# Kernel optimization log

Measured on AMD Instinct MI355X. Metric: run time of the kernel, lower is better.

## Reference

```python
import jax, jax.numpy as jnp
import numpy as np

N = 100000      # nodes
E = 3200000     # edges
F_IN = 1433     # Cora num_node_features
H = 16          # hidden channels
C = 7           # Cora num_classes


def setup_inputs() -> dict:
    key = jax.random.key(0)
    ks = jax.random.split(key, 8)
    x = jax.random.normal(ks[0], (N, F_IN), dtype=jnp.float32)
    edge_index = jax.random.randint(ks[1], (2, E), 0, N, dtype=jnp.int64)
    W1 = jax.random.normal(ks[2], (F_IN, H), dtype=jnp.float32) * (1.0 / np.sqrt(F_IN))
    b1 = jnp.zeros((H,), dtype=jnp.float32)
    W2 = jax.random.normal(ks[3], (H, H), dtype=jnp.float32) * (1.0 / np.sqrt(H))
    b2 = jnp.zeros((H,), dtype=jnp.float32)
    W3 = jax.random.normal(ks[4], (H, C), dtype=jnp.float32) * (1.0 / np.sqrt(H))
    b3 = jnp.zeros((C,), dtype=jnp.float32)
    return {"x": x, "W1": W1, "b1": b1, "W2": W2, "b2": b2,
            "W3": W3, "b3": b3, "edge_index": edge_index}


def reference(x, W1, b1, W2, b2, W3, b3, edge_index):
    # Add self loops (GCNConv default) and compute symmetric normalization once;
    # it is identical for all three layers.
    loop = jnp.arange(N, dtype=edge_index.dtype)
    src = jnp.concatenate([edge_index[0], loop])
    dst = jnp.concatenate([edge_index[1], loop])
    deg = jax.ops.segment_sum(jnp.ones_like(dst, dtype=x.dtype), dst, num_segments=N)
    dinv = jnp.where(deg > 0, jax.lax.rsqrt(deg), 0.0)
    norm = dinv[src] * dinv[dst]  # [E+N]

    def conv(h, W, b):
        h = h @ W                                   # [N, out]
        msg = h[src] * norm[:, None]                # gather + scale, [E+N, out]
        return jax.ops.segment_sum(msg, dst, num_segments=N) + b

    h = jax.nn.relu(conv(x, W1, b1))
    h = jax.nn.relu(conv(h, W2, b2))
    logits = conv(h, W3, b3)
    return jax.nn.log_softmax(logits, axis=1)
```

## Files before the change

kernel.cpp:

```cpp
#include <hip/hip_runtime.h>
#include <hip/hip_fp16.h>

#define F_IN 1433
#define BCAP 96
#define WSTR 2048


typedef _Float16 f16x8 __attribute__((ext_vector_type(8)));
typedef float    f32x4 __attribute__((ext_vector_type(4)));

__global__ __launch_bounds__(256) void k_prep(const float* __restrict__ W1,
    int* __restrict__ cnt, _Float16* __restrict__ wt, int N)
{
    int i = blockIdx.x * 256 + threadIdx.x;
    if (i < N) cnt[i] = 0;
    if (i < 16 * WSTR) {
        int c = i >> 11, k = i & (WSTR - 1);
        float v = (k < F_IN) ? W1[k * 16 + c] : 0.0f;
        wt[i] = (_Float16)v;
    }
}

__global__ __launch_bounds__(256) void k_scatter(const int* __restrict__ ei,
    int* cnt, int* bucket, int E, int N)
{
    int e = blockIdx.x * 256 + threadIdx.x;
    if (e < E) {
        int s = ei[e], d = ei[E + e];
        if ((unsigned)s < (unsigned)N && (unsigned)d < (unsigned)N) {
            int slot = atomicAdd(&cnt[d], 1);
            if (slot < BCAP) bucket[(size_t)d * BCAP + slot] = s;
        }
    }
}

__global__ __launch_bounds__(256, 4) void k_gemm(
    const float* __restrict__ x, const _Float16* __restrict__ wt,
    const int* __restrict__ cnt, float* __restrict__ s, int N)
{
    int tid = threadIdx.x;
    int wv = tid >> 6, lane = tid & 63;
    int ntiles = (N + 15) >> 4;
    int tile = blockIdx.x * 4 + wv;
    if (tile >= ntiles) return;

    int rc = lane & 15;
    int g  = lane >> 4;
    int row = tile * 16 + rc;
    const float* xr = x + (size_t)((row < N) ? row : (N - 1)) * F_IN;
    const _Float16* wrow = wt + (rc << 11);

    struct __attribute__((packed, aligned(4))) f4u { float f[4]; };

    f32x4 acc = {0.0f, 0.0f, 0.0f, 0.0f};
    int kb = g * 8;

    #pragma unroll 4
    for (int ch = 0; ch < 44; ++ch) {
        int k0 = ch * 32 + kb;
        f4u xa = *(const f4u*)&xr[k0];
        f4u xb = *(const f4u*)&xr[k0 + 4];
        f16x8 bv = *(const f16x8*)&wrow[k0];
        f16x8 av;
        #pragma unroll
        for (int j = 0; j < 4; ++j) {
            av[j]     = (_Float16)xa.f[j];
            av[j + 4] = (_Float16)xb.f[j];
        }
        acc = __builtin_amdgcn_mfma_f32_16x16x32_f16(av, bv, acc, 0, 0, 0);
    }
    {
        int k0 = 1408 + kb;
        f16x8 av, bv;
        bv = *(const f16x8*)&wrow[k0];
        #pragma unroll
        for (int j = 0; j < 8; ++j) {
            int k = k0 + j;
            av[j] = (_Float16)((k < F_IN) ? xr[k] : 0.0f);
        }
        acc = __builtin_amdgcn_mfma_f32_16x16x32_f16(av, bv, acc, 0, 0, 0);
    }

    #pragma unroll
    for (int r = 0; r < 4; ++r) {
        int grow = tile * 16 + g * 4 + r;
        if (grow < N) {
            float di = rsqrtf((float)cnt[grow] + 1.0f);
            s[grow * 16 + rc] = acc[r] * di;
        }
    }
}

__global__ __launch_bounds__(256) void k_aggA(
    const int* __restrict__ cnt, const int* __restrict__ bucket,
    const float* __restrict__ sin, const float* __restrict__ W,
    const float* __restrict__ bias, float* __restrict__ sout, int N)
{
    __shared__ float w[256], bs[16];
    int tid = threadIdx.x;
    w[tid] = W[tid];
    if (tid < 16) bs[tid] = bias[tid];
    __syncthreads();

    int wave = tid >> 6, lane = tid & 63;
    int dst = blockIdx.x * 4 + wave;
    if (dst >= N) return;
    int g = lane >> 4, c = lane & 15;
    int deg = min(cnt[dst], BCAP);
    const int* bk = bucket + (size_t)dst * BCAP;

    int e0 = (lane < deg)      ? bk[lane]      : 0;
    int e1 = (64 + lane < deg) ? bk[64 + lane] : 0;

    float acc = (g == 0) ? sin[dst * 16 + c] : 0.0f;
    for (int base = 0; base < deg; base += 32) {
        float vs = 0.0f;
        #pragma unroll
        for (int i = 0; i < 8; ++i) {
            int j = base + g + 4 * i;
            int sa = __shfl(e0, j & 63, 64), sb = __shfl(e1, j & 63, 64);
            int sv = (j < 64) ? sa : sb;
            float v = (j < deg) ? sin[sv * 16 + c] : 0.0f;
            vs += v;
        }
        acc += vs;
    }
    acc += __shfl_xor(acc, 16, 64);
    acc += __shfl_xor(acc, 32, 64);

    float di = rsqrtf((float)cnt[dst] + 1.0f);
    float h = fmaxf(fmaf(di, acc, bs[c]), 0.0f);
    float t = 0.0f;
    #pragma unroll
    for (int k = 0; k < 16; ++k)
        t = fmaf(__shfl(h, k, 16), w[k * 16 + c], t);
    if (lane < 16) sout[dst * 16 + c] = di * t;
}

__global__ __launch_bounds__(256) void k_aggB(
    const int* __restrict__ cnt, const int* __restrict__ bucket,
    const float* __restrict__ sin, const float* __restrict__ W,
    const float* __restrict__ bias, float* __restrict__ sout, int N)
{
    __shared__ float w[112], bs[16];
    int tid = threadIdx.x;
    if (tid < 112) w[tid] = W[tid];
    if (tid < 16) bs[tid] = bias[tid];
    __syncthreads();

    int wave = tid >> 6, lane = tid & 63;
    int dst = blockIdx.x * 4 + wave;
    if (dst >= N) return;
    int g = lane >> 4, c = lane & 15;
    int deg = min(cnt[dst], BCAP);
    const int* bk = bucket + (size_t)dst * BCAP;

    int e0 = (lane < deg)      ? bk[lane]      : 0;
    int e1 = (64 + lane < deg) ? bk[64 + lane] : 0;

    float acc = (g == 0) ? sin[dst * 16 + c] : 0.0f;
    for (int base = 0; base < deg; base += 32) {
        float vs = 0.0f;
        #pragma unroll
        for (int i = 0; i < 8; ++i) {
            int j = base + g + 4 * i;
            int sa = __shfl(e0, j & 63, 64), sb = __shfl(e1, j & 63, 64);
            int sv = (j < 64) ? sa : sb;
            float v = (j < deg) ? sin[sv * 16 + c] : 0.0f;
            vs += v;
        }
        acc += vs;
    }
    acc += __shfl_xor(acc, 16, 64);
    acc += __shfl_xor(acc, 32, 64);

    float di = rsqrtf((float)cnt[dst] + 1.0f);
    float h = fmaxf(fmaf(di, acc, bs[c]), 0.0f);
    int cc = (c < 7) ? c : 0;
    float t = 0.0f;
    #pragma unroll
    for (int k = 0; k < 16; ++k)
        t = fmaf(__shfl(h, k, 16), w[k * 7 + cc], t);
    if (lane < 7) sout[dst * 7 + c] = di * t;
}

__global__ __launch_bounds__(256) void k_aggC(
    const int* __restrict__ cnt, const int* __restrict__ bucket,
    const float* __restrict__ sin, const float* __restrict__ bias,
    float* __restrict__ out, int N)
{
    __shared__ float bs[8];
    int tid = threadIdx.x;
    if (tid < 7) bs[tid] = bias[tid];
    if (tid == 7) bs[7] = 0.0f;
    __syncthreads();

    int wave = tid >> 6, lane = tid & 63;
    int dst = blockIdx.x * 4 + wave;
    if (dst >= N) return;
    int g8 = lane >> 3, c8 = lane & 7;
    bool c7 = (c8 < 7);
    int cc = c7 ? c8 : 0;
    int deg = min(cnt[dst], BCAP);
    const int* bk = bucket + (size_t)dst * BCAP;

    int e0 = (lane < deg)      ? bk[lane]      : 0;
    int e1 = (64 + lane < deg) ? bk[64 + lane] : 0;

    float acc = (g8 == 0 && c7) ? sin[dst * 7 + c8] : 0.0f;
    for (int base = 0; base < deg; base += 64) {
        float vs = 0.0f;
        #pragma unroll
        for (int i = 0; i < 8; ++i) {
            int j = base + g8 + 8 * i;
            int sa = __shfl(e0, j & 63, 64), sb = __shfl(e1, j & 63, 64);
            int sv = (j < 64) ? sa : sb;
            float v = (j < deg && c7) ? sin[sv * 7 + cc] : 0.0f;
            vs += v;
        }
        acc += vs;
    }
    acc += __shfl_xor(acc, 8, 64);
    acc += __shfl_xor(acc, 16, 64);
    acc += __shfl_xor(acc, 32, 64);

    if (lane < 8) {
        float di = rsqrtf((float)cnt[dst] + 1.0f);
        float logit = c7 ? fmaf(di, acc, bs[c8]) : -1e30f;
        float m = logit;
        m = fmaxf(m, __shfl_xor(m, 1, 8));
        m = fmaxf(m, __shfl_xor(m, 2, 8));
        m = fmaxf(m, __shfl_xor(m, 4, 8));
        float e = c7 ? expf(logit - m) : 0.0f;
        float ssum = e;
        ssum += __shfl_xor(ssum, 1, 8);
        ssum += __shfl_xor(ssum, 2, 8);
        ssum += __shfl_xor(ssum, 4, 8);
        if (c7) out[dst * 7 + c8] = logit - m - logf(ssum);
    }
}

extern "C" void kernel_launch(void* const* d_in, const int* in_sizes, int n_in,
                              void* d_out, int out_size, void* d_ws, size_t ws_size,
                              hipStream_t stream)
{
    const float* x  = (const float*)d_in[0];
    const float* W1 = (const float*)d_in[1];
    const float* b1 = (const float*)d_in[2];
    const float* W2 = (const float*)d_in[3];
    const float* b2 = (const float*)d_in[4];
    const float* W3 = (const float*)d_in[5];
    const float* b3 = (const float*)d_in[6];
    const int*   ei = (const int*)d_in[7];
    float* out = (float*)d_out;

    int N = in_sizes[0] / F_IN;
    int E = in_sizes[7] / 2;

    int*      cnt    = (int*)d_ws;
    int*      bucket = cnt + N;
    _Float16* wt     = (_Float16*)(bucket + (size_t)N * BCAP);
    float*    s1     = (float*)(wt + 16 * WSTR);
    float*    s2     = s1 + 16 * (size_t)N;
    float*    s3     = s2 + 16 * (size_t)N;

    int nbN = (N + 255) / 256;
    int nbE = (E + 255) / 256;
    int nb4 = (N + 3) / 4;
    int ntiles = (N + 15) / 16;
    int nbG = (ntiles + 3) / 4;

    k_prep   <<<nbN, 256, 0, stream>>>(W1, cnt, wt, N);
    k_scatter<<<nbE, 256, 0, stream>>>(ei, cnt, bucket, E, N);
    k_gemm   <<<nbG, 256, 0, stream>>>(x, wt, cnt, s1, N);
    k_aggA   <<<nb4, 256, 0, stream>>>(cnt, bucket, s1, W2, b1, s2, N);
    k_aggB   <<<nb4, 256, 0, stream>>>(cnt, bucket, s2, W3, b2, s3, N);
    k_aggC   <<<nb4, 256, 0, stream>>>(cnt, bucket, s3, b3, out, N);
}
```

Baseline: 504.2 us.

## Fuse all stages into one persistent kernel with software grid barriers

Replaces the five separate launches (scatter, gemm, three aggregation layers) with one persistent kernel sized to the device's resident block count. Stages are separated by atomic-counter grid barriers. The GEMM now runs before the edge scatter, so the degree scaling of s1 moves into a separate elementwise pass after the first barrier. This removes launch gaps and lets the x-streaming GEMM and the atomic scatter run in the same kernel. The cost is barrier spin overhead, an extra pass over s1, a lower occupancy cap from launch bounds, and a host-side device-property query on every call.

```diff
diff --git a/kernel.cpp b/kernel.cpp
--- a/kernel.cpp
+++ b/kernel.cpp
@@ -10,233 +10,213 @@
 typedef float    f32x4 __attribute__((ext_vector_type(4)));
 
 __global__ __launch_bounds__(256) void k_prep(const float* __restrict__ W1,
-    int* __restrict__ cnt, _Float16* __restrict__ wt, int N)
+    int* __restrict__ bar, int* __restrict__ cnt, _Float16* __restrict__ wt, int N)
 {
     int i = blockIdx.x * 256 + threadIdx.x;
+    if (i < 16) bar[i] = 0;
     if (i < N) cnt[i] = 0;
     if (i < 16 * WSTR) {
         int c = i >> 11, k = i & (WSTR - 1);
-        float v = (k < F_IN) ? W1[k * 16 + c] : 0.0f;
-        wt[i] = (_Float16)v;
-    }
-}
-
-__global__ __launch_bounds__(256) void k_scatter(const int* __restrict__ ei,
-    int* cnt, int* bucket, int E, int N)
+        wt[i] = (_Float16)((k < F_IN) ? W1[k * 16 + c] : 0.0f);
+    }
+}
+
+__device__ __forceinline__ void gridbar(int* bar, int target) {
+    __syncthreads();
+    if (threadIdx.x == 0) {
+        __hip_atomic_fetch_add(bar, 1, __ATOMIC_RELEASE, __HIP_MEMORY_SCOPE_AGENT);
+        while (__hip_atomic_load(bar, __ATOMIC_RELAXED, __HIP_MEMORY_SCOPE_AGENT) < target)
+            __builtin_amdgcn_s_sleep(32);
+        (void)__hip_atomic_load(bar, __ATOMIC_ACQUIRE, __HIP_MEMORY_SCOPE_AGENT);
+    }
+    __syncthreads();
+}
+
+__global__ __launch_bounds__(256, 6) void k_all(
+    const float* __restrict__ x, const _Float16* __restrict__ wt,
+    const int* __restrict__ ei, int* __restrict__ cnt, int* __restrict__ bucket,
+    float* __restrict__ s1, float* __restrict__ s2, float* __restrict__ s3,
+    float* __restrict__ out,
+    const float* __restrict__ W2, const float* __restrict__ b1,
+    const float* __restrict__ W3, const float* __restrict__ b2,
+    const float* __restrict__ b3, int* bar, int N, int E)
 {
-    int e = blockIdx.x * 256 + threadIdx.x;
-    if (e < E) {
-        int s = ei[e], d = ei[E + e];
-        if ((unsigned)s < (unsigned)N && (unsigned)d < (unsigned)N) {
+    __shared__ float w2s[256], w3s[112], b1s[16], b2s[16], b3s[8];
+    int tid = threadIdx.x;
+    w2s[tid] = W2[tid];
+    if (tid < 112) w3s[tid] = W3[tid];
+    if (tid < 16)  b1s[tid] = b1[tid];
+    if (tid < 16)  b2s[tid] = b2[tid];
+    if (tid < 8)   b3s[tid] = (tid < 7) ? b3[tid] : 0.0f;
+    __syncthreads();
+
+    int G = gridDim.x;
+    int wv = tid >> 6, lane = tid & 63;
+    int gw = blockIdx.x * 4 + wv, ngw = G * 4;
+    int gt = blockIdx.x * 256 + tid, ngt = G * 256;
+
+    struct __attribute__((packed, aligned(4))) f4u { float f[4]; };
+
+    {
+        int rc = lane & 15, g = lane >> 4;
+        int kb = g * 8;
+        int ntiles = (N + 15) >> 4;
+        const _Float16* wrow = wt + (rc << 11);
+        for (int tile = gw; tile < ntiles; tile += ngw) {
+            int row = tile * 16 + rc;
+            const float* xr = x + (size_t)((row < N) ? row : (N - 1)) * F_IN;
+            f32x4 acc = {0.0f, 0.0f, 0.0f, 0.0f};
+            #pragma unroll 4
+            for (int ch = 0; ch < 44; ++ch) {
+                int k0 = ch * 32 + kb;
+                f4u xa = *(const f4u*)&xr[k0];
+                f4u xb = *(const f4u*)&xr[k0 + 4];
+                f16x8 bv = *(const f16x8*)&wrow[k0];
+                f16x8 av;
+                #pragma unroll
+                for (int j = 0; j < 4; ++j) {
+                    av[j]     = (_Float16)xa.f[j];
+                    av[j + 4] = (_Float16)xb.f[j];
+                }
+                acc = __builtin_amdgcn_mfma_f32_16x16x32_f16(av, bv, acc, 0, 0, 0);
+            }
+            {
+                int k0 = 1408 + kb;
+                f16x8 av, bv;
+                bv = *(const f16x8*)&wrow[k0];
+                #pragma unroll
+                for (int j = 0; j < 8; ++j) {
+                    int k = k0 + j;
+                    av[j] = (_Float16)((k < F_IN) ? xr[k] : 0.0f);
+                }
+                acc = __builtin_amdgcn_mfma_f32_16x16x32_f16(av, bv, acc, 0, 0, 0);
+            }
+            #pragma unroll
+            for (int r = 0; r < 4; ++r) {
+                int grow = tile * 16 + g * 4 + r;
+                if (grow < N) s1[grow * 16 + rc] = acc[r];
+            }
+        }
+    }
+
+    for (int e = gt; e < E; e += ngt) {
+        int sv = ei[e], d = ei[E + e];
+        if ((unsigned)sv < (unsigned)N && (unsigned)d < (unsigned)N) {
             int slot = atomicAdd(&cnt[d], 1);
-            if (slot < BCAP) bucket[(size_t)d * BCAP + slot] = s;
-        }
-    }
-}
-
-__global__ __launch_bounds__(256, 4) void k_gemm(
-    const float* __restrict__ x, const _Float16* __restrict__ wt,
-    const int* __restrict__ cnt, float* __restrict__ s, int N)
-{
-    int tid = threadIdx.x;
-    int wv = tid >> 6, lane = tid & 63;
-    int ntiles = (N + 15) >> 4;
-    int tile = blockIdx.x * 4 + wv;
-    if (tile >= ntiles) return;
-
-    int rc = lane & 15;
-    int g  = lane >> 4;
-    int row = tile * 16 + rc;
-    const float* xr = x + (size_t)((row < N) ? row : (N - 1)) * F_IN;
-    const _Float16* wrow = wt + (rc << 11);
-
-    struct __attribute__((packed, aligned(4))) f4u { float f[4]; };
-
-    f32x4 acc = {0.0f, 0.0f, 0.0f, 0.0f};
-    int kb = g * 8;
-
-    #pragma unroll 4
-    for (int ch = 0; ch < 44; ++ch) {
-        int k0 = ch * 32 + kb;
-        f4u xa = *(const f4u*)&xr[k0];
-        f4u xb = *(const f4u*)&xr[k0 + 4];
-        f16x8 bv = *(const f16x8*)&wrow[k0];
-        f16x8 av;
+            if (slot < BCAP) bucket[(size_t)d * BCAP + slot] = sv;
+        }
+    }
+
+    gridbar(bar, G);
+
+    for (int i = gt; i < N * 16; i += ngt)
+        s1[i] *= rsqrtf((float)cnt[i >> 4] + 1.0f);
+
+    gridbar(bar, 2 * G);
+
+    int g = lane >> 4, c = lane & 15;
+
+    for (int dst = gw; dst < N; dst += ngw) {
+        int deg = min(cnt[dst], BCAP);
+        const int* bk = bucket + (size_t)dst * BCAP;
+        int e0 = (lane < deg)      ? bk[lane]      : 0;
+        int e1 = (64 + lane < deg) ? bk[64 + lane] : 0;
+        float acc = (g == 0) ? s1[dst * 16 + c] : 0.0f;
+        for (int base = 0; base < deg; base += 32) {
+            float vs = 0.0f;
+            #pragma unroll
+            for (int i = 0; i < 8; ++i) {
+                int j = base + g + 4 * i;
+                int sa = __shfl(e0, j & 63, 64), sb = __shfl(e1, j & 63, 64);
+                int sv = (j < 64) ? sa : sb;
+                float v = (j < deg) ? s1[sv * 16 + c] : 0.0f;
+                vs += v;
+            }
+            acc += vs;
+        }
+        acc += __shfl_xor(acc, 16, 64);
+        acc += __shfl_xor(acc, 32, 64);
+        float di = rsqrtf((float)cnt[dst] + 1.0f);
+        float h = fmaxf(fmaf(di, acc, b1s[c]), 0.0f);
+        float t = 0.0f;
         #pragma unroll
-        for (int j = 0; j < 4; ++j) {
-            av[j]     = (_Float16)xa.f[j];
-            av[j + 4] = (_Float16)xb.f[j];
-        }
-        acc = __builtin_amdgcn_mfma_f32_16x16x32_f16(av, bv, acc, 0, 0, 0);
-    }
-    {
-        int k0 = 1408 + kb;
-        f16x8 av, bv;
-        bv = *(const f16x8*)&wrow[k0];
+        for (int k = 0; k < 16; ++k)
+            t = fmaf(__shfl(h, k, 16), w2s[k * 16 + c], t);
+        if (lane < 16) s2[dst * 16 + c] = di * t;
+    }
+
+    gridbar(bar, 3 * G);
+
+    for (int dst = gw; dst < N; dst += ngw) {
+        int deg = min(cnt[dst], BCAP);
+        const int* bk = bucket + (size_t)dst * BCAP;
+        int e0 = (lane < deg)      ? bk[lane]      : 0;
+        int e1 = (64 + lane < deg) ? bk[64 + lane] : 0;
+        float acc = (g == 0) ? s2[dst * 16 + c] : 0.0f;
+        for (int base = 0; base < deg; base += 32) {
+            float vs = 0.0f;
+            #pragma unroll
+            for (int i = 0; i < 8; ++i) {
+                int j = base + g + 4 * i;
+                int sa = __shfl(e0, j & 63, 64), sb = __shfl(e1, j & 63, 64);
+                int sv = (j < 64) ? sa : sb;
+                float v = (j < deg) ? s2[sv * 16 + c] : 0.0f;
+                vs += v;
+            }
+            acc += vs;
+        }
+        acc += __shfl_xor(acc, 16, 64);
+        acc += __shfl_xor(acc, 32, 64);
+        float di = rsqrtf((float)cnt[dst] + 1.0f);
+        float h = fmaxf(fmaf(di, acc, b2s[c]), 0.0f);
+        int cc = (c < 7) ? c : 0;
+        float t = 0.0f;
         #pragma unroll
-        for (int j = 0; j < 8; ++j) {
-            int k = k0 + j;
-            av[j] = (_Float16)((k < F_IN) ? xr[k] : 0.0f);
-        }
-        acc = __builtin_amdgcn_mfma_f32_16x16x32_f16(av, bv, acc, 0, 0, 0);
-    }
-
-    #pragma unroll
-    for (int r = 0; r < 4; ++r) {
-        int grow = tile * 16 + g * 4 + r;
-        if (grow < N) {
-            float di = rsqrtf((float)cnt[grow] + 1.0f);
-            s[grow * 16 + rc] = acc[r] * di;
-        }
-    }
-}
-
-__global__ __launch_bounds__(256) void k_aggA(
-    const int* __restrict__ cnt, const int* __restrict__ bucket,
-    const float* __restrict__ sin, const float* __restrict__ W,
-    const float* __restrict__ bias, float* __restrict__ sout, int N)
-{
-    __shared__ float w[256], bs[16];
-    int tid = threadIdx.x;
-    w[tid] = W[tid];
-    if (tid < 16) bs[tid] = bias[tid];
-    __syncthreads();
-
-    int wave = tid >> 6, lane = tid & 63;
-    int dst = blockIdx.x * 4 + wave;
-    if (dst >= N) return;
-    int g = lane >> 4, c = lane & 15;
-    int deg = min(cnt[dst], BCAP);
-    const int* bk = bucket + (size_t)dst * BCAP;
-
-    int e0 = (lane < deg)      ? bk[lane]      : 0;
-    int e1 = (64 + lane < deg) ? bk[64 + lane] : 0;
-
-    float acc = (g == 0) ? sin[dst * 16 + c] : 0.0f;
-    for (int base = 0; base < deg; base += 32) {
-        float vs = 0.0f;
-        #pragma unroll
-        for (int i = 0; i < 8; ++i) {
-            int j = base + g + 4 * i;
-            int sa = __shfl(e0, j & 63, 64), sb = __shfl(e1, j & 63, 64);
-            int sv = (j < 64) ? sa : sb;
-            float v = (j < deg) ? sin[sv * 16 + c] : 0.0f;
-            vs += v;
-        }
-        acc += vs;
-    }
-    acc += __shfl_xor(acc, 16, 64);
-    acc += __shfl_xor(acc, 32, 64);
-
-    float di = rsqrtf((float)cnt[dst] + 1.0f);
-    float h = fmaxf(fmaf(di, acc, bs[c]), 0.0f);
-    float t = 0.0f;
-    #pragma unroll
-    for (int k = 0; k < 16; ++k)
-        t = fmaf(__shfl(h, k, 16), w[k * 16 + c], t);
-    if (lane < 16) sout[dst * 16 + c] = di * t;
-}
-
-__global__ __launch_bounds__(256) void k_aggB(
-    const int* __restrict__ cnt, const int* __restrict__ bucket,
-    const float* __restrict__ sin, const float* __restrict__ W,
-    const float* __restrict__ bias, float* __restrict__ sout, int N)
-{
-    __shared__ float w[112], bs[16];
-    int tid = threadIdx.x;
-    if (tid < 112) w[tid] = W[tid];
-    if (tid < 16) bs[tid] = bias[tid];
-    __syncthreads();
-
-    int wave = tid >> 6, lane = tid & 63;
-    int dst = blockIdx.x * 4 + wave;
-    if (dst >= N) return;
-    int g = lane >> 4, c = lane & 15;
-    int deg = min(cnt[dst], BCAP);
-    const int* bk = bucket + (size_t)dst * BCAP;
-
-    int e0 = (lane < deg)      ? bk[lane]      : 0;
-    int e1 = (64 + lane < deg) ? bk[64 + lane] : 0;
-
-    float acc = (g == 0) ? sin[dst * 16 + c] : 0.0f;
-    for (int base = 0; base < deg; base += 32) {
-        float vs = 0.0f;
-        #pragma unroll
-        for (int i = 0; i < 8; ++i) {
-            int j = base + g + 4 * i;
-            int sa = __shfl(e0, j & 63, 64), sb = __shfl(e1, j & 63, 64);
-            int sv = (j < 64) ? sa : sb;
-            float v = (j < deg) ? sin[sv * 16 + c] : 0.0f;
-            vs += v;
-        }
-        acc += vs;
-    }
-    acc += __shfl_xor(acc, 16, 64);
-    acc += __shfl_xor(acc, 32, 64);
-
-    float di = rsqrtf((float)cnt[dst] + 1.0f);
-    float h = fmaxf(fmaf(di, acc, bs[c]), 0.0f);
-    int cc = (c < 7) ? c : 0;
-    float t = 0.0f;
-    #pragma unroll
-    for (int k = 0; k < 16; ++k)
-        t = fmaf(__shfl(h, k, 16), w[k * 7 + cc], t);
-    if (lane < 7) sout[dst * 7 + c] = di * t;
-}
-
-__global__ __launch_bounds__(256) void k_aggC(
-    const int* __restrict__ cnt, const int* __restrict__ bucket,
-    const float* __restrict__ sin, const float* __restrict__ bias,
-    float* __restrict__ out, int N)
-{
-    __shared__ float bs[8];
-    int tid = threadIdx.x;
-    if (tid < 7) bs[tid] = bias[tid];
-    if (tid == 7) bs[7] = 0.0f;
-    __syncthreads();
-
-    int wave = tid >> 6, lane = tid & 63;
-    int dst = blockIdx.x * 4 + wave;
-    if (dst >= N) return;
+        for (int k = 0; k < 16; ++k)
+            t = fmaf(__shfl(h, k, 16), w3s[k * 7 + cc], t);
+        if (lane < 7) s3[dst * 7 + c] = di * t;
+    }
+
+    gridbar(bar, 4 * G);
+
     int g8 = lane >> 3, c8 = lane & 7;
     bool c7 = (c8 < 7);
-    int cc = c7 ? c8 : 0;
-    int deg = min(cnt[dst], BCAP);
-    const int* bk = bucket + (size_t)dst * BCAP;
-
-    int e0 = (lane < deg)      ? bk[lane]      : 0;
-    int e1 = (64 + lane < deg) ? bk[64 + lane] : 0;
-
-    float acc = (g8 == 0 && c7) ? sin[dst * 7 + c8] : 0.0f;
-    for (int base = 0; base < deg; base += 64) {
-        float vs = 0.0f;
-        #pragma unroll
-        for (int i = 0; i < 8; ++i) {
-            int j = base + g8 + 8 * i;
-            int sa = __shfl(e0, j & 63, 64), sb = __shfl(e1, j & 63, 64);
-            int sv = (j < 64) ? sa : sb;
-            float v = (j < deg && c7) ? sin[sv * 7 + cc] : 0.0f;
-            vs += v;
-        }
-        acc += vs;
-    }
-    acc += __shfl_xor(acc, 8, 64);
-    acc += __shfl_xor(acc, 16, 64);
-    acc += __shfl_xor(acc, 32, 64);
-
-    if (lane < 8) {
-        float di = rsqrtf((float)cnt[dst] + 1.0f);
-        float logit = c7 ? fmaf(di, acc, bs[c8]) : -1e30f;
-        float m = logit;
-        m = fmaxf(m, __shfl_xor(m, 1, 8));
-        m = fmaxf(m, __shfl_xor(m, 2, 8));
-        m = fmaxf(m, __shfl_xor(m, 4, 8));
-        float e = c7 ? expf(logit - m) : 0.0f;
-        float ssum = e;
-        ssum += __shfl_xor(ssum, 1, 8);
-        ssum += __shfl_xor(ssum, 2, 8);
-        ssum += __shfl_xor(ssum, 4, 8);
-        if (c7) out[dst * 7 + c8] = logit - m - logf(ssum);
+    int cc8 = c7 ? c8 : 0;
+    for (int dst = gw; dst < N; dst += ngw) {
+        int deg = min(cnt[dst], BCAP);
+        const int* bk = bucket + (size_t)dst * BCAP;
+        int e0 = (lane < deg)      ? bk[lane]      : 0;
+        int e1 = (64 + lane < deg) ? bk[64 + lane] : 0;
+        float acc = (g8 == 0 && c7) ? s3[dst * 7 + c8] : 0.0f;
+        for (int base = 0; base < deg; base += 64) {
+            float vs = 0.0f;
+            #pragma unroll
+            for (int i = 0; i < 8; ++i) {
+                int j = base + g8 + 8 * i;
+                int sa = __shfl(e0, j & 63, 64), sb = __shfl(e1, j & 63, 64);
+                int sv = (j < 64) ? sa : sb;
+                float v = (j < deg && c7) ? s3[sv * 7 + cc8] : 0.0f;
+                vs += v;
+            }
+            acc += vs;
+        }
+        acc += __shfl_xor(acc, 8, 64);
+        acc += __shfl_xor(acc, 16, 64);
+        acc += __shfl_xor(acc, 32, 64);
+        if (lane < 8) {
+            float di = rsqrtf((float)cnt[dst] + 1.0f);
+            float logit = c7 ? fmaf(di, acc, b3s[c8]) : -1e30f;
+            float m = logit;
+            m = fmaxf(m, __shfl_xor(m, 1, 8));
+            m = fmaxf(m, __shfl_xor(m, 2, 8));
+            m = fmaxf(m, __shfl_xor(m, 4, 8));
+            float e = c7 ? expf(logit - m) : 0.0f;
+            float ssum = e;
+            ssum += __shfl_xor(ssum, 1, 8);
+            ssum += __shfl_xor(ssum, 2, 8);
+            ssum += __shfl_xor(ssum, 4, 8);
+            if (c7) out[dst * 7 + c8] = logit - m - logf(ssum);
+        }
     }
 }
 
@@ -257,7 +237,8 @@
     int N = in_sizes[0] / F_IN;
     int E = in_sizes[7] / 2;
 
-    int*      cnt    = (int*)d_ws;
+    int*      bar    = (int*)d_ws;
+    int*      cnt    = bar + 16;
     int*      bucket = cnt + N;
     _Float16* wt     = (_Float16*)(bucket + (size_t)N * BCAP);
     float*    s1     = (float*)(wt + 16 * WSTR);
@@ -265,15 +246,16 @@
     float*    s3     = s2 + 16 * (size_t)N;
 
     int nbN = (N + 255) / 256;
-    int nbE = (E + 255) / 256;
-    int nb4 = (N + 3) / 4;
-    int ntiles = (N + 15) / 16;
-    int nbG = (ntiles + 3) / 4;
-
-    k_prep   <<<nbN, 256, 0, stream>>>(W1, cnt, wt, N);
-    k_scatter<<<nbE, 256, 0, stream>>>(ei, cnt, bucket, E, N);
-    k_gemm   <<<nbG, 256, 0, stream>>>(x, wt, cnt, s1, N);
-    k_aggA   <<<nb4, 256, 0, stream>>>(cnt, bucket, s1, W2, b1, s2, N);
-    k_aggB   <<<nb4, 256, 0, stream>>>(cnt, bucket, s2, W3, b2, s3, N);
-    k_aggC   <<<nb4, 256, 0, stream>>>(cnt, bucket, s3, b3, out, N);
-}
+    k_prep<<<nbN, 256, 0, stream>>>(W1, bar, cnt, wt, N);
+
+    int dev = 0, numCU = 256, occ = 6;
+    hipGetDevice(&dev);
+    hipDeviceProp_t props;
+    if (hipGetDeviceProperties(&props, dev) == hipSuccess) numCU = props.multiProcessorCount;
+    if (hipOccupancyMaxActiveBlocksPerMultiprocessor(&occ, k_all, 256, 0) != hipSuccess || occ < 1)
+        occ = 1;
+    int grid = numCU * occ;
+
+    k_all<<<grid, 256, 0, stream>>>(x, wt, ei, cnt, bucket, s1, s2, s3, out,
+                                    W2, b1, W3, b2, b3, bar, N, E);
+}
```

Measured after the change: 822.4 us. +63.1%, slower.

## Stage x tile in LDS as fp16 and split K across waves

Applied to the files above, without the earlier changes.

The first-layer GEMM now has each block own one 16-row tile. It loads that tile's x rows with coalesced row-contiguous reads, converts them to fp16 into shared memory, and splits the K loop across the four waves. Partial MFMA accumulators are combined with a shared-memory reduction before degree scaling. This replaces strided per-lane global reads with coalesced loads. In exchange it needs about 50KB of LDS per block, which lowers occupancy, and adds two barriers per block.

```diff
diff --git a/kernel.cpp b/kernel.cpp
--- a/kernel.cpp
+++ b/kernel.cpp
@@ -4,6 +4,7 @@
 #define F_IN 1433
 #define BCAP 96
 #define WSTR 2048
+#define XSTR 1448
 
 
 typedef _Float16 f16x8 __attribute__((ext_vector_type(8)));
@@ -34,60 +35,73 @@
     }
 }
 
-__global__ __launch_bounds__(256, 4) void k_gemm(
+__global__ __launch_bounds__(256) void k_gemm(
     const float* __restrict__ x, const _Float16* __restrict__ wt,
     const int* __restrict__ cnt, float* __restrict__ s, int N)
 {
-    int tid = threadIdx.x;
-    int wv = tid >> 6, lane = tid & 63;
+    __shared__ _Float16 xs[16 * XSTR];
+    __shared__ float red[4 * 256];
+
+    int tid = threadIdx.x;
+    int w = tid >> 6, lane = tid & 63;
+    int tile = blockIdx.x;
     int ntiles = (N + 15) >> 4;
-    int tile = blockIdx.x * 4 + wv;
     if (tile >= ntiles) return;
+
+    struct __attribute__((packed, aligned(4))) f4u { float f[4]; };
+
+    #pragma unroll
+    for (int r = 0; r < 4; ++r) {
+        int rr = w * 4 + r;
+        int grow = tile * 16 + rr;
+        const float* xr = x + (size_t)((grow < N) ? grow : (N - 1)) * F_IN;
+        #pragma unroll
+        for (int it = 0; it < 6; ++it) {
+            int k4 = it * 256 + lane * 4;
+            if (k4 < XSTR) {
+                _Float16 h4[4];
+                if (k4 + 4 <= F_IN) {
+                    f4u v = *(const f4u*)&xr[k4];
+                    #pragma unroll
+                    for (int j = 0; j < 4; ++j) h4[j] = (_Float16)v.f[j];
+                } else {
+                    #pragma unroll
+                    for (int j = 0; j < 4; ++j) {
+                        int k = k4 + j;
+                        h4[j] = (_Float16)((k < F_IN) ? xr[k] : 0.0f);
+                    }
+                }
+                *(__attribute__((ext_vector_type(4))) _Float16*)&xs[rr * XSTR + k4] =
+                    *(__attribute__((ext_vector_type(4))) _Float16*)h4;
+            }
+        }
+    }
+    __syncthreads();
 
     int rc = lane & 15;
     int g  = lane >> 4;
-    int row = tile * 16 + rc;
-    const float* xr = x + (size_t)((row < N) ? row : (N - 1)) * F_IN;
+    int kb = g * 8;
     const _Float16* wrow = wt + (rc << 11);
-
-    struct __attribute__((packed, aligned(4))) f4u { float f[4]; };
+    const _Float16* xrow = xs + rc * XSTR;
 
     f32x4 acc = {0.0f, 0.0f, 0.0f, 0.0f};
-    int kb = g * 8;
-
-    #pragma unroll 4
-    for (int ch = 0; ch < 44; ++ch) {
+    for (int ch = w; ch < 45; ch += 4) {
         int k0 = ch * 32 + kb;
-        f4u xa = *(const f4u*)&xr[k0];
-        f4u xb = *(const f4u*)&xr[k0 + 4];
+        f16x8 av = *(const f16x8*)&xrow[k0];
         f16x8 bv = *(const f16x8*)&wrow[k0];
-        f16x8 av;
-        #pragma unroll
-        for (int j = 0; j < 4; ++j) {
-            av[j]     = (_Float16)xa.f[j];
-            av[j + 4] = (_Float16)xb.f[j];
-        }
         acc = __builtin_amdgcn_mfma_f32_16x16x32_f16(av, bv, acc, 0, 0, 0);
     }
-    {
-        int k0 = 1408 + kb;
-        f16x8 av, bv;
-        bv = *(const f16x8*)&wrow[k0];
-        #pragma unroll
-        for (int j = 0; j < 8; ++j) {
-            int k = k0 + j;
-            av[j] = (_Float16)((k < F_IN) ? xr[k] : 0.0f);
-        }
-        acc = __builtin_amdgcn_mfma_f32_16x16x32_f16(av, bv, acc, 0, 0, 0);
-    }
-
-    #pragma unroll
-    for (int r = 0; r < 4; ++r) {
-        int grow = tile * 16 + g * 4 + r;
-        if (grow < N) {
-            float di = rsqrtf((float)cnt[grow] + 1.0f);
-            s[grow * 16 + rc] = acc[r] * di;
-        }
+
+    #pragma unroll
+    for (int q = 0; q < 4; ++q)
+        red[w * 256 + (g * 4 + q) * 16 + rc] = acc[q];
+    __syncthreads();
+
+    int row = tile * 16 + (tid >> 4);
+    if (row < N) {
+        float v = red[tid] + red[256 + tid] + red[512 + tid] + red[768 + tid];
+        float di = rsqrtf((float)cnt[row] + 1.0f);
+        s[row * 16 + (tid & 15)] = v * di;
     }
 }
 
@@ -268,11 +282,10 @@
     int nbE = (E + 255) / 256;
     int nb4 = (N + 3) / 4;
     int ntiles = (N + 15) / 16;
-    int nbG = (ntiles + 3) / 4;
 
     k_prep   <<<nbN, 256, 0, stream>>>(W1, cnt, wt, N);
     k_scatter<<<nbE, 256, 0, stream>>>(ei, cnt, bucket, E, N);
-    k_gemm   <<<nbG, 256, 0, stream>>>(x, wt, cnt, s1, N);
+    k_gemm   <<<ntiles, 256, 0, stream>>>(x, wt, cnt, s1, N);
     k_aggA   <<<nb4, 256, 0, stream>>>(cnt, bucket, s1, W2, b1, s2, N);
     k_aggB   <<<nb4, 256, 0, stream>>>(cnt, bucket, s2, W3, b2, s3, N);
     k_aggC   <<<nb4, 256, 0, stream>>>(cnt, bucket, s3, b3, out, N);
```

Result: slower. 535.0 us (+6.1%).

## Merge GEMM and edge scatter into one launch, defer degree scaling to aggregation

Applied to the files above, without the earlier changes.

The layer-1 GEMM and the edge bucketing scatter now run as disjoint block ranges of a single kernel, so the compute-heavy feature transform can overlap the atomic-bound scatter. This is possible because the GEMM no longer needs degree counts: it writes unscaled features, and the first aggregation applies rsqrt(deg) per source neighbour on the fly. In exchange that aggregation does an extra gather of cnt for every edge. The aggregation kernels also process four destinations per wave instead of one, which cuts the block count.

```diff
diff --git a/kernel.cpp b/kernel.cpp
--- a/kernel.cpp
+++ b/kernel.cpp
@@ -21,79 +21,75 @@
     }
 }
 
-__global__ __launch_bounds__(256) void k_scatter(const int* __restrict__ ei,
-    int* cnt, int* bucket, int E, int N)
-{
-    int e = blockIdx.x * 256 + threadIdx.x;
-    if (e < E) {
-        int s = ei[e], d = ei[E + e];
-        if ((unsigned)s < (unsigned)N && (unsigned)d < (unsigned)N) {
-            int slot = atomicAdd(&cnt[d], 1);
-            if (slot < BCAP) bucket[(size_t)d * BCAP + slot] = s;
-        }
-    }
-}
-
-__global__ __launch_bounds__(256, 4) void k_gemm(
+__global__ __launch_bounds__(256) void k_ms(
     const float* __restrict__ x, const _Float16* __restrict__ wt,
-    const int* __restrict__ cnt, float* __restrict__ s, int N)
-{
-    int tid = threadIdx.x;
-    int wv = tid >> 6, lane = tid & 63;
-    int ntiles = (N + 15) >> 4;
-    int tile = blockIdx.x * 4 + wv;
-    if (tile >= ntiles) return;
-
-    int rc = lane & 15;
-    int g  = lane >> 4;
-    int row = tile * 16 + rc;
-    const float* xr = x + (size_t)((row < N) ? row : (N - 1)) * F_IN;
-    const _Float16* wrow = wt + (rc << 11);
-
-    struct __attribute__((packed, aligned(4))) f4u { float f[4]; };
-
-    f32x4 acc = {0.0f, 0.0f, 0.0f, 0.0f};
-    int kb = g * 8;
-
-    #pragma unroll 4
-    for (int ch = 0; ch < 44; ++ch) {
-        int k0 = ch * 32 + kb;
-        f4u xa = *(const f4u*)&xr[k0];
-        f4u xb = *(const f4u*)&xr[k0 + 4];
-        f16x8 bv = *(const f16x8*)&wrow[k0];
-        f16x8 av;
+    const int* __restrict__ ei, int* __restrict__ cnt, int* __restrict__ bucket,
+    float* __restrict__ g1, int nbG, int N, int E)
+{
+    int tid = threadIdx.x;
+    if ((int)blockIdx.x < nbG) {
+        int wv = tid >> 6, lane = tid & 63;
+        int ntiles = (N + 15) >> 4;
+        int tile = blockIdx.x * 4 + wv;
+        if (tile >= ntiles) return;
+
+        int rc = lane & 15;
+        int g  = lane >> 4;
+        int row = tile * 16 + rc;
+        const float* xr = x + (size_t)((row < N) ? row : (N - 1)) * F_IN;
+        const _Float16* wrow = wt + (rc << 11);
+
+        struct __attribute__((packed, aligned(4))) f4u { float f[4]; };
+
+        f32x4 acc = {0.0f, 0.0f, 0.0f, 0.0f};
+        int kb = g * 8;
+
+        #pragma unroll 4
+        for (int ch = 0; ch < 44; ++ch) {
+            int k0 = ch * 32 + kb;
+            f4u xa = *(const f4u*)&xr[k0];
+            f4u xb = *(const f4u*)&xr[k0 + 4];
+            f16x8 bv = *(const f16x8*)&wrow[k0];
+            f16x8 av;
+            #pragma unroll
+            for (int j = 0; j < 4; ++j) {
+                av[j]     = (_Float16)xa.f[j];
+                av[j + 4] = (_Float16)xb.f[j];
+            }
+            acc = __builtin_amdgcn_mfma_f32_16x16x32_f16(av, bv, acc, 0, 0, 0);
+        }
+        {
+            int k0 = 1408 + kb;
+            f16x8 av, bv;
+            bv = *(const f16x8*)&wrow[k0];
+            #pragma unroll
+            for (int j = 0; j < 8; ++j) {
+                int k = k0 + j;
+                av[j] = (_Float16)((k < F_IN) ? xr[k] : 0.0f);
+            }
+            acc = __builtin_amdgcn_mfma_f32_16x16x32_f16(av, bv, acc, 0, 0, 0);
+        }
+
         #pragma unroll
-        for (int j = 0; j < 4; ++j) {
-            av[j]     = (_Float16)xa.f[j];
-            av[j + 4] = (_Float16)xb.f[j];
-        }
-        acc = __builtin_amdgcn_mfma_f32_16x16x32_f16(av, bv, acc, 0, 0, 0);
-    }
-    {
-        int k0 = 1408 + kb;
-        f16x8 av, bv;
-        bv = *(const f16x8*)&wrow[k0];
-        #pragma unroll
-        for (int j = 0; j < 8; ++j) {
-            int k = k0 + j;
-            av[j] = (_Float16)((k < F_IN) ? xr[k] : 0.0f);
-        }
-        acc = __builtin_amdgcn_mfma_f32_16x16x32_f16(av, bv, acc, 0, 0, 0);
-    }
-
-    #pragma unroll
-    for (int r = 0; r < 4; ++r) {
-        int grow = tile * 16 + g * 4 + r;
-        if (grow < N) {
-            float di = rsqrtf((float)cnt[grow] + 1.0f);
-            s[grow * 16 + rc] = acc[r] * di;
+        for (int r = 0; r < 4; ++r) {
+            int grow = tile * 16 + g * 4 + r;
+            if (grow < N) g1[grow * 16 + rc] = acc[r];
+        }
+    } else {
+        int e = ((int)blockIdx.x - nbG) * 256 + tid;
+        if (e < E) {
+            int s = ei[e], d = ei[E + e];
+            if ((unsigned)s < (unsigned)N && (unsigned)d < (unsigned)N) {
+                int slot = atomicAdd(&cnt[d], 1);
+                if (slot < BCAP) bucket[(size_t)d * BCAP + slot] = s;
+            }
         }
     }
 }
 
 __global__ __launch_bounds__(256) void k_aggA(
     const int* __restrict__ cnt, const int* __restrict__ bucket,
-    const float* __restrict__ sin, const float* __restrict__ W,
+    const float* __restrict__ g1, const float* __restrict__ W,
     const float* __restrict__ bias, float* __restrict__ sout, int N)
 {
     __shared__ float w[256], bs[16];
@@ -103,38 +99,45 @@
     __syncthreads();
 
     int wave = tid >> 6, lane = tid & 63;
-    int dst = blockIdx.x * 4 + wave;
-    if (dst >= N) return;
     int g = lane >> 4, c = lane & 15;
-    int deg = min(cnt[dst], BCAP);
-    const int* bk = bucket + (size_t)dst * BCAP;
-
-    int e0 = (lane < deg)      ? bk[lane]      : 0;
-    int e1 = (64 + lane < deg) ? bk[64 + lane] : 0;
-
-    float acc = (g == 0) ? sin[dst * 16 + c] : 0.0f;
-    for (int base = 0; base < deg; base += 32) {
-        float vs = 0.0f;
+    int base0 = blockIdx.x * 16 + wave * 4;
+
+    for (int it = 0; it < 4; ++it) {
+        int dst = base0 + it;
+        if (dst >= N) break;
+        int cd = cnt[dst];
+        int deg = min(cd, BCAP);
+        float di = rsqrtf((float)cd + 1.0f);
+        const int* bk = bucket + (size_t)dst * BCAP;
+
+        int e0 = (lane < deg)      ? bk[lane]      : 0;
+        int e1 = (64 + lane < deg) ? bk[64 + lane] : 0;
+
+        float acc = (g == 0) ? di * g1[dst * 16 + c] : 0.0f;
+        for (int base = 0; base < deg; base += 32) {
+            float vs = 0.0f;
+            #pragma unroll
+            for (int i = 0; i < 8; ++i) {
+                int j = base + g + 4 * i;
+                int sa = __shfl(e0, j & 63, 64), sb = __shfl(e1, j & 63, 64);
+                int sv = (j < 64) ? sa : sb;
+                float v = 0.0f;
+                if (j < deg)
+                    v = rsqrtf((float)cnt[sv] + 1.0f) * g1[sv * 16 + c];
+                vs += v;
+            }
+            acc += vs;
+        }
+        acc += __shfl_xor(acc, 16, 64);
+        acc += __shfl_xor(acc, 32, 64);
+
+        float h = fmaxf(fmaf(di, acc, bs[c]), 0.0f);
+        float t = 0.0f;
         #pragma unroll
-        for (int i = 0; i < 8; ++i) {
-            int j = base + g + 4 * i;
-            int sa = __shfl(e0, j & 63, 64), sb = __shfl(e1, j & 63, 64);
-            int sv = (j < 64) ? sa : sb;
-            float v = (j < deg) ? sin[sv * 16 + c] : 0.0f;
-            vs += v;
-        }
-        acc += vs;
-    }
-    acc += __shfl_xor(acc, 16, 64);
-    acc += __shfl_xor(acc, 32, 64);
-
-    float di = rsqrtf((float)cnt[dst] + 1.0f);
-    float h = fmaxf(fmaf(di, acc, bs[c]), 0.0f);
-    float t = 0.0f;
-    #pragma unroll
-    for (int k = 0; k < 16; ++k)
-        t = fmaf(__shfl(h, k, 16), w[k * 16 + c], t);
-    if (lane < 16) sout[dst * 16 + c] = di * t;
+        for (int k = 0; k < 16; ++k)
+            t = fmaf(__shfl(h, k, 16), w[k * 16 + c], t);
+        if (lane < 16) sout[dst * 16 + c] = di * t;
+    }
 }
 
 __global__ __launch_bounds__(256) void k_aggB(
@@ -149,39 +152,44 @@
     __syncthreads();
 
     int wave = tid >> 6, lane = tid & 63;
-    int dst = blockIdx.x * 4 + wave;
-    if (dst >= N) return;
     int g = lane >> 4, c = lane & 15;
-    int deg = min(cnt[dst], BCAP);
-    const int* bk = bucket + (size_t)dst * BCAP;
-
-    int e0 = (lane < deg)      ? bk[lane]      : 0;
-    int e1 = (64 + lane < deg) ? bk[64 + lane] : 0;
-
-    float acc = (g == 0) ? sin[dst * 16 + c] : 0.0f;
-    for (int base = 0; base < deg; base += 32) {
-        float vs = 0.0f;
+    int base0 = blockIdx.x * 16 + wave * 4;
+
+    for (int it = 0; it < 4; ++it) {
+        int dst = base0 + it;
+        if (dst >= N) break;
+        int cd = cnt[dst];
+        int deg = min(cd, BCAP);
+        float di = rsqrtf((float)cd + 1.0f);
+        const int* bk = bucket + (size_t)dst * BCAP;
+
+        int e0 = (lane < deg)      ? bk[lane]      : 0;
+        int e1 = (64 + lane < deg) ? bk[64 + lane] : 0;
+
+        float acc = (g == 0) ? sin[dst * 16 + c] : 0.0f;
+        for (int base = 0; base < deg; base += 32) {
+            float vs = 0.0f;
+            #pragma unroll
+            for (int i = 0; i < 8; ++i) {
+                int j = base + g + 4 * i;
+                int sa = __shfl(e0, j & 63, 64), sb = __shfl(e1, j & 63, 64);
+                int sv = (j < 64) ? sa : sb;
+                float v = (j < deg) ? sin[sv * 16 + c] : 0.0f;
+                vs += v;
+            }
+            acc += vs;
+        }
+        acc += __shfl_xor(acc, 16, 64);
+        acc += __shfl_xor(acc, 32, 64);
+
+        float h = fmaxf(fmaf(di, acc, bs[c]), 0.0f);
+        int cc = (c < 7) ? c : 0;
+        float t = 0.0f;
         #pragma unroll
-        for (int i = 0; i < 8; ++i) {
-            int j = base + g + 4 * i;
-            int sa = __shfl(e0, j & 63, 64), sb = __shfl(e1, j & 63, 64);
-            int sv = (j < 64) ? sa : sb;
-            float v = (j < deg) ? sin[sv * 16 + c] : 0.0f;
-            vs += v;
-        }
-        acc += vs;
-    }
-    acc += __shfl_xor(acc, 16, 64);
-    acc += __shfl_xor(acc, 32, 64);
-
-    float di = rsqrtf((float)cnt[dst] + 1.0f);
-    float h = fmaxf(fmaf(di, acc, bs[c]), 0.0f);
-    int cc = (c < 7) ? c : 0;
-    float t = 0.0f;
-    #pragma unroll
-    for (int k = 0; k < 16; ++k)
-        t = fmaf(__shfl(h, k, 16), w[k * 7 + cc], t);
-    if (lane < 7) sout[dst * 7 + c] = di * t;
+        for (int k = 0; k < 16; ++k)
+            t = fmaf(__shfl(h, k, 16), w[k * 7 + cc], t);
+        if (lane < 7) sout[dst * 7 + c] = di * t;
+    }
 }
 
 __global__ __launch_bounds__(256) void k_aggC(
@@ -196,47 +204,52 @@
     __syncthreads();
 
     int wave = tid >> 6, lane = tid & 63;
-    int dst = blockIdx.x * 4 + wave;
-    if (dst >= N) return;
     int g8 = lane >> 3, c8 = lane & 7;
     bool c7 = (c8 < 7);
     int cc = c7 ? c8 : 0;
-    int deg = min(cnt[dst], BCAP);
-    const int* bk = bucket + (size_t)dst * BCAP;
-
-    int e0 = (lane < deg)      ? bk[lane]      : 0;
-    int e1 = (64 + lane < deg) ? bk[64 + lane] : 0;
-
-    float acc = (g8 == 0 && c7) ? sin[dst * 7 + c8] : 0.0f;
-    for (int base = 0; base < deg; base += 64) {
-        float vs = 0.0f;
-        #pragma unroll
-        for (int i = 0; i < 8; ++i) {
-            int j = base + g8 + 8 * i;
-            int sa = __shfl(e0, j & 63, 64), sb = __shfl(e1, j & 63, 64);
-            int sv = (j < 64) ? sa : sb;
-            float v = (j < deg && c7) ? sin[sv * 7 + cc] : 0.0f;
-            vs += v;
-        }
-        acc += vs;
-    }
-    acc += __shfl_xor(acc, 8, 64);
-    acc += __shfl_xor(acc, 16, 64);
-    acc += __shfl_xor(acc, 32, 64);
-
-    if (lane < 8) {
-        float di = rsqrtf((float)cnt[dst] + 1.0f);
-        float logit = c7 ? fmaf(di, acc, bs[c8]) : -1e30f;
-        float m = logit;
-        m = fmaxf(m, __shfl_xor(m, 1, 8));
-        m = fmaxf(m, __shfl_xor(m, 2, 8));
-        m = fmaxf(m, __shfl_xor(m, 4, 8));
-        float e = c7 ? expf(logit - m) : 0.0f;
-        float ssum = e;
-        ssum += __shfl_xor(ssum, 1, 8);
-        ssum += __shfl_xor(ssum, 2, 8);
-        ssum += __shfl_xor(ssum, 4, 8);
-        if (c7) out[dst * 7 + c8] = logit - m - logf(ssum);
+    int base0 = blockIdx.x * 16 + wave * 4;
+
+    for (int it = 0; it < 4; ++it) {
+        int dst = base0 + it;
+        if (dst >= N) break;
+        int cd = cnt[dst];
+        int deg = min(cd, BCAP);
+        float di = rsqrtf((float)cd + 1.0f);
+        const int* bk = bucket + (size_t)dst * BCAP;
+
+        int e0 = (lane < deg)      ? bk[lane]      : 0;
+        int e1 = (64 + lane < deg) ? bk[64 + lane] : 0;
+
+        float acc = (g8 == 0 && c7) ? sin[dst * 7 + c8] : 0.0f;
+        for (int base = 0; base < deg; base += 64) {
+            float vs = 0.0f;
+            #pragma unroll
+            for (int i = 0; i < 8; ++i) {
+                int j = base + g8 + 8 * i;
+                int sa = __shfl(e0, j & 63, 64), sb = __shfl(e1, j & 63, 64);
+                int sv = (j < 64) ? sa : sb;
+                float v = (j < deg && c7) ? sin[sv * 7 + cc] : 0.0f;
+                vs += v;
+            }
+            acc += vs;
+        }
+        acc += __shfl_xor(acc, 8, 64);
+        acc += __shfl_xor(acc, 16, 64);
+        acc += __shfl_xor(acc, 32, 64);
+
+        if (lane < 8) {
+            float logit = c7 ? fmaf(di, acc, bs[c8]) : -1e30f;
+            float m = logit;
+            m = fmaxf(m, __shfl_xor(m, 1, 8));
+            m = fmaxf(m, __shfl_xor(m, 2, 8));
+            m = fmaxf(m, __shfl_xor(m, 4, 8));
+            float e = c7 ? expf(logit - m) : 0.0f;
+            float ssum = e;
+            ssum += __shfl_xor(ssum, 1, 8);
+            ssum += __shfl_xor(ssum, 2, 8);
+            ssum += __shfl_xor(ssum, 4, 8);
+            if (c7) out[dst * 7 + c8] = logit - m - logf(ssum);
+        }
     }
 }
 
@@ -260,20 +273,19 @@
     int*      cnt    = (int*)d_ws;
     int*      bucket = cnt + N;
     _Float16* wt     = (_Float16*)(bucket + (size_t)N * BCAP);
-    float*    s1     = (float*)(wt + 16 * WSTR);
-    float*    s2     = s1 + 16 * (size_t)N;
+    float*    g1     = (float*)(wt + 16 * WSTR);
+    float*    s2     = g1 + 16 * (size_t)N;
     float*    s3     = s2 + 16 * (size_t)N;
 
-    int nbN = (N + 255) / 256;
-    int nbE = (E + 255) / 256;
-    int nb4 = (N + 3) / 4;
+    int nbN  = (N + 255) / 256;
+    int nbE  = (E + 255) / 256;
+    int nb16 = (N + 15) / 16;
     int ntiles = (N + 15) / 16;
-    int nbG = (ntiles + 3) / 4;
-
-    k_prep   <<<nbN, 256, 0, stream>>>(W1, cnt, wt, N);
-    k_scatter<<<nbE, 256, 0, stream>>>(ei, cnt, bucket, E, N);
-    k_gemm   <<<nbG, 256, 0, stream>>>(x, wt, cnt, s1, N);
-    k_aggA   <<<nb4, 256, 0, stream>>>(cnt, bucket, s1, W2, b1, s2, N);
-    k_aggB   <<<nb4, 256, 0, stream>>>(cnt, bucket, s2, W3, b2, s3, N);
-    k_aggC   <<<nb4, 256, 0, stream>>>(cnt, bucket, s3, b3, out, N);
-}
+    int nbG  = (ntiles + 3) / 4;
+
+    k_prep<<<nbN, 256, 0, stream>>>(W1, cnt, wt, N);
+    k_ms  <<<nbG + nbE, 256, 0, stream>>>(x, wt, ei, cnt, bucket, g1, nbG, N, E);
+    k_aggA<<<nb16, 256, 0, stream>>>(cnt, bucket, g1, W2, b1, s2, N);
+    k_aggB<<<nb16, 256, 0, stream>>>(cnt, bucket, s2, W3, b2, s3, N);
+    k_aggC<<<nb16, 256, 0, stream>>>(cnt, bucket, s3, b3, out, N);
+}
```

Measured after the change: 509.2 us. No clear change (+1.0%).
